# Kernel tuning notes

Hardware: AMD Instinct MI355X
Metric: run time of the kernel (lower is better)

## Reference

```python
import jax, jax.numpy as jnp
import numpy as np

HIDDEN = 2048
N_HEADS = 32
N_KV_HEADS = 8
HEAD_DIM = 64
ROPE_THETA = 500000.0
B, S = 1, 2048


def _rope_tables(seq_len):
    inv_freq = 1.0 / ROPE_THETA ** (jnp.arange(0, HEAD_DIM, 2, dtype=jnp.float32) / HEAD_DIM)
    angles = jnp.arange(seq_len, dtype=jnp.float32)[:, None] * inv_freq[None, :]
    return jnp.cos(angles), jnp.sin(angles)


def _apply_rope(x, cos, sin):
    # x: (B, S, H, D); cos/sin: (S, D//2)
    x1 = x[..., 0::2]
    x2 = x[..., 1::2]
    c = cos[None, :, None, :]
    s = sin[None, :, None, :]
    x1r = x1 * c - x2 * s
    x2r = x1 * s + x2 * c
    return jnp.stack([x1r, x2r], axis=-1).reshape(x.shape)


def setup_inputs() -> dict:
    key = jax.random.key(0)
    ks = jax.random.split(key, 5)
    hidden_states = jax.random.normal(ks[0], (B, S, HIDDEN), dtype=jnp.float32)
    # causal mask, broadcastable over (B, H, S, S)
    attention_mask = jnp.tril(jnp.ones((S, S), dtype=bool))[None, :, :]
    sc = 1.0 / np.sqrt(HIDDEN)
    wq = jax.random.normal(ks[1], (HIDDEN, N_HEADS * HEAD_DIM), dtype=jnp.float32) * sc
    wk = jax.random.normal(ks[2], (HIDDEN, N_KV_HEADS * HEAD_DIM), dtype=jnp.float32) * sc
    wv = jax.random.normal(ks[3], (HIDDEN, N_KV_HEADS * HEAD_DIM), dtype=jnp.float32) * sc
    wo = jax.random.normal(ks[4], (N_HEADS * HEAD_DIM, HIDDEN), dtype=jnp.float32) * sc
    return {"hidden_states": hidden_states, "attention_mask": attention_mask,
            "wq": wq, "wk": wk, "wv": wv, "wo": wo}


def reference(hidden_states, attention_mask, wq, wk, wv, wo):
    b, s, _ = hidden_states.shape
    groups = N_HEADS // N_KV_HEADS
    q = (hidden_states @ wq).reshape(b, s, N_HEADS, HEAD_DIM)
    k = (hidden_states @ wk).reshape(b, s, N_KV_HEADS, HEAD_DIM)
    v = (hidden_states @ wv).reshape(b, s, N_KV_HEADS, HEAD_DIM)
    cos, sin = _rope_tables(s)
    q = _apply_rope(q, cos, sin)
    k = _apply_rope(k, cos, sin)
    k = jnp.repeat(k, groups, axis=2)  # (b, s, H, D)
    v = jnp.repeat(v, groups, axis=2)
    q = q.transpose(0, 2, 1, 3)  # (b, H, s, D)
    k = k.transpose(0, 2, 1, 3)
    v = v.transpose(0, 2, 1, 3)
    scores = jnp.einsum('bhqd,bhkd->bhqk', q, k) / jnp.sqrt(jnp.float32(HEAD_DIM))
    scores = jnp.where(attention_mask[:, None, :, :], scores, -jnp.inf)
    probs = jax.nn.softmax(scores, axis=-1)
    out = jnp.einsum('bhqk,bhkd->bhqd', probs, v)
    out = out.transpose(0, 2, 1, 3).reshape(b, s, N_HEADS * HEAD_DIM)
    return out @ wo
```

## Files before the change

kernel.cpp:

```cpp
#include <hip/hip_runtime.h>

typedef __attribute__((ext_vector_type(8))) short short8;
typedef __attribute__((ext_vector_type(4))) float float4v;

union U4S8 { uint4 u; short8 s; };

__device__ __forceinline__ float bf2f(ushort u) {
    union { uint i; float f; } v; v.i = ((uint)u) << 16; return v.f;
}
__device__ __forceinline__ ushort f2bf(float f) {
    union { uint i; float f; } v; v.f = f;
    return (ushort)((v.i + 0x7FFFu + ((v.i >> 16) & 1u)) >> 16);
}
#if __has_builtin(__builtin_amdgcn_cvt_pk_bf16_f32)
__device__ __forceinline__ uint f2bf_pk(float a, float b) {
    auto r = __builtin_amdgcn_cvt_pk_bf16_f32(a, b);
    return __builtin_bit_cast(uint, r);
}
#else
__device__ __forceinline__ uint f2bf_pk(float a, float b) {
    return (uint)f2bf(a) | ((uint)f2bf(b) << 16);
}
#endif
__device__ __forceinline__ void gld_lds16(const ushort* g, ushort* l) {
    __builtin_amdgcn_global_load_lds((const __attribute__((address_space(1))) unsigned int*)g,
                                     (__attribute__((address_space(3))) unsigned int*)l,
                                     16, 0, 0);
}

__device__ __forceinline__ void tconv_body(const float* in, ushort* out,
                                           int C, int r0, int c0, int tid) {
    __shared__ float t[64][65];
    const int lrow = tid >> 2;
    const int lc   = (tid & 3) * 16;
    const float* ip = in + (size_t)(r0 + lrow) * C + c0 + lc;
#pragma unroll
    for (int i = 0; i < 4; i++) {
        float4 v = *(const float4*)(ip + 4 * i);
        t[lrow][lc + 4 * i + 0] = v.x; t[lrow][lc + 4 * i + 1] = v.y;
        t[lrow][lc + 4 * i + 2] = v.z; t[lrow][lc + 4 * i + 3] = v.w;
    }
    __syncthreads();
    ushort* op = out + (size_t)(c0 + lrow) * 2048 + r0 + lc;
#pragma unroll
    for (int i = 0; i < 8; i++)
        ((uint*)op)[i] = f2bf_pk(t[lc + 2 * i][lrow], t[lc + 2 * i + 1][lrow]);
}

__global__ __launch_bounds__(256) void prep(const float* __restrict__ hidden,
                                            const float* __restrict__ wq,
                                            const float* __restrict__ wk,
                                            const float* __restrict__ wv,
                                            const float* __restrict__ wo,
                                            ushort* __restrict__ hid,
                                            ushort* __restrict__ wT,
                                            ushort* __restrict__ woT) {
    const int bx = blockIdx.x;
    if (bx < 2048) {
        const size_t i = ((size_t)bx * 256 + threadIdx.x) * 8;
        float4 a = *(const float4*)(hidden + i);
        float4 b = *(const float4*)(hidden + i + 4);
        uint4 u;
        u.x = f2bf_pk(a.x, a.y); u.y = f2bf_pk(a.z, a.w);
        u.z = f2bf_pk(b.x, b.y); u.w = f2bf_pk(b.z, b.w);
        *(uint4*)(hid + i) = u;
    } else if (bx < 3584) {
        const int i = bx - 2048;
        const int xx = i % 48, yy = i / 48;
        const float* in; ushort* op; int C, cx;
        if (xx < 32)      { in = wq; op = wT;                        C = 2048; cx = xx; }
        else if (xx < 40) { in = wk; op = wT + (size_t)2048 * 2048;  C = 512;  cx = xx - 32; }
        else              { in = wv; op = wT + (size_t)2560 * 2048;  C = 512;  cx = xx - 40; }
        tconv_body(in, op, C, yy * 64, cx * 64, threadIdx.x);
    } else {
        const int i = bx - 3584;
        tconv_body(wo, woT, 2048, (i >> 5) * 64, (i & 31) * 64, threadIdx.x);
    }
}

template <bool BF16OUT>
__global__ __launch_bounds__(512, 2) void gemm_n128(const ushort* __restrict__ A,
                                                    const ushort* __restrict__ Bt,
                                                    void* __restrict__ Cout,
                                                    int N, int K, int lda, int ropeQKV,
                                                    ushort* __restrict__ VTout) {
    __shared__ ushort As[2][2][128 * 32];
    __shared__ ushort Bs[2][2][128 * 32];

    const int tid = threadIdx.x, w = tid >> 6, lane = tid & 63;
    const int lr = lane & 15, quad = lane >> 4;
    const int m0 = blockIdx.x * 128, n0 = blockIdx.y * 128;
    const int wr = w >> 1, wc = w & 1;

    const int srow = lane >> 2;
    const int skb  = (lane & 3) ^ ((srow >> 1) & 3);

    const ushort* Ap = A  + (size_t)(m0 + 16 * w + srow) * lda + skb * 8;
    const ushort* Bp = Bt + (size_t)(n0 + 16 * w + srow) * K + skb * 8;

    float4v acc[2][4];
#pragma unroll
    for (int a = 0; a < 2; a++)
#pragma unroll
        for (int b = 0; b < 4; b++) { acc[a][b][0] = 0.f; acc[a][b][1] = 0.f; acc[a][b][2] = 0.f; acc[a][b][3] = 0.f; }

    const int fsw = (lr >> 1) & 3;
    const int niter = K >> 6;

    gld_lds16(Ap,      &As[0][0][w * 512]);
    gld_lds16(Ap + 32, &As[0][1][w * 512]);
    gld_lds16(Bp,      &Bs[0][0][w * 512]);
    gld_lds16(Bp + 32, &Bs[0][1][w * 512]);

    for (int it = 0; it < niter; it++) {
        const int b = it & 1;

        asm volatile("s_waitcnt vmcnt(0) lgkmcnt(0)\n\ts_barrier" ::: "memory");

        if (it + 1 < niter) {
            const int k1 = (it + 1) << 6;
            gld_lds16(Ap + k1,      &As[1 - b][0][w * 512]);
            gld_lds16(Ap + k1 + 32, &As[1 - b][1][w * 512]);
            gld_lds16(Bp + k1,      &Bs[1 - b][0][w * 512]);
            gld_lds16(Bp + k1 + 32, &Bs[1 - b][1][w * 512]);
        }

#pragma unroll
        for (int kh = 0; kh < 2; kh++) {
            short8 af[2], bf[4];
#pragma unroll
            for (int mt = 0; mt < 2; mt++)
                af[mt] = *(const short8*)&As[b][kh][(wr * 32 + mt * 16 + lr) * 32 + (quad ^ fsw) * 8];
#pragma unroll
            for (int nt = 0; nt < 4; nt++)
                bf[nt] = *(const short8*)&Bs[b][kh][(wc * 64 + nt * 16 + lr) * 32 + (quad ^ fsw) * 8];
#pragma unroll
            for (int mt = 0; mt < 2; mt++)
#pragma unroll
                for (int nt = 0; nt < 4; nt++)
                    acc[mt][nt] = __builtin_amdgcn_mfma_f32_16x16x32_bf16(af[mt], bf[nt], acc[mt][nt], 0, 0, 0);
        }
    }

    const int rbase = m0 + wr * 32 + quad * 4;
    const int cbase = n0 + wc * 64 + lr;
    if (BF16OUT) {
        ushort* Cb = (ushort*)Cout;
        if (ropeQKV && (int)blockIdx.y >= 20) {
            const int ch = rbase >> 6;
            const int j2 = (wr & 1) * 2;
#pragma unroll
            for (int nt = 0; nt < 4; nt++) {
                const int vd = cbase + nt * 16 - 2560;
                const int vx = vd & 15;
#pragma unroll
                for (int r = 0; r < 4; r++) {
                    const int kl = quad * 4 + r;
                    const uint pk = f2bf_pk(acc[0][nt][r], acc[1][nt][r]);
                    *(uint*)(VTout + (size_t)vd * 2048 + ch * 64
                             + ((kl ^ vx) << 2) + j2) = pk;
                }
            }
        } else if (ropeQKV && (int)blockIdx.y < 20) {
            const float osc = ((int)blockIdx.y < 16) ? 0.18033688f : 1.0f;
            const float sgn = (lr & 1) ? 1.0f : -1.0f;
#pragma unroll
            for (int nt = 0; nt < 4; nt++) {
                const int col = cbase + nt * 16;
                const int j = (col >> 1) & 31;
                const float inv = __expf(-(float)(2 * j) * (1.0f / 64.0f) * 13.122363377404328f);
#pragma unroll
                for (int mt = 0; mt < 2; mt++)
#pragma unroll
                    for (int r = 0; r < 4; r++) {
                        const int row = rbase + mt * 16 + r;
                        float sn, cs;
                        sincosf((float)row * inv, &sn, &cs);
                        const float mine = acc[mt][nt][r];
                        const float partner = __shfl_xor(mine, 1);
                        Cb[(size_t)row * N + col] = f2bf((mine * cs + sgn * partner * sn) * osc);
                    }
            }
        } else {
#pragma unroll
            for (int mt = 0; mt < 2; mt++)
#pragma unroll
                for (int nt = 0; nt < 4; nt++)
#pragma unroll
                    for (int r = 0; r < 4; r++)
                        Cb[(size_t)(rbase + mt * 16 + r) * N + cbase + nt * 16] = f2bf(acc[mt][nt][r]);
        }
    } else {
        float* Cf = (float*)Cout;
#pragma unroll
        for (int mt = 0; mt < 2; mt++)
#pragma unroll
            for (int nt = 0; nt < 4; nt++)
#pragma unroll
                for (int r = 0; r < 4; r++)
                    Cf[(size_t)(rbase + mt * 16 + r) * N + cbase + nt * 16] = acc[mt][nt][r];
    }
}

__global__ __launch_bounds__(256) void attn_mfma(const ushort* __restrict__ Q,
                                                 const ushort* __restrict__ Kc,
                                                 const ushort* __restrict__ VT,
                                                 ushort* __restrict__ O0,
                                                 ushort* __restrict__ O1,
                                                 float* __restrict__ L0,
                                                 float* __restrict__ L1) {
    __shared__ ushort Ks[2][64 * 64];
    __shared__ ushort Vt[2][64 * 64];
    __shared__ ushort Ps[4][16 * 64];

    const int tid = threadIdx.x, w = tid >> 6, lane = tid & 63;
    const int lr = lane & 15, quad = lane >> 4;
    const int h = blockIdx.y, g = h >> 2, z = blockIdx.z;

    const int ksub = lane >> 3, dsub = lane & 7;
    ushort* Pw = Ps[w];
    ushort* Op = z ? O1 : O0;
    float*  Lp = z ? L1 : L0;

    const ushort* Kp0 = Kc + g * 64 + ((dsub ^ ksub) * 8) + (size_t)3072 * ksub;
    const ushort* Vp0 = VT + (size_t)(g * 64 + ksub) * 2048 + dsub * 8;

    short8 onesf;
#pragma unroll
    for (int j = 0; j < 8; j++) onesf[j] = (short)0x3F80;

    for (int ti = 0; ti < 2; ti++) {
        const int bx = ti ? 31 - (int)blockIdx.x : (int)blockIdx.x;
        const int nch = (bx >= z) ? ((bx - z) >> 1) + 1 : 0;

        const ushort* qp = Q + (size_t)(bx * 64 + w * 16 + lr) * 3072 + h * 64 + quad * 8;
        const short8 qf0 = *(const short8*)qp;
        const short8 qf1 = *(const short8*)(qp + 32);

        float4v oacc[4], lacc;
#pragma unroll
        for (int t = 0; t < 4; t++) { oacc[t][0] = 0.f; oacc[t][1] = 0.f; oacc[t][2] = 0.f; oacc[t][3] = 0.f; }
        lacc[0] = 0.f; lacc[1] = 0.f; lacc[2] = 0.f; lacc[3] = 0.f;

        __syncthreads();
        if (nch) {
#pragma unroll
            for (int i = 0; i < 2; i++) {
                const int rt = 2 * w + i;
                gld_lds16(Kp0 + (size_t)(z * 64 + rt * 8) * 3072, &Ks[0][rt * 512]);
                gld_lds16(Vp0 + (size_t)(rt * 8) * 2048 + z * 64, &Vt[0][rt * 512]);
            }
        }

        for (int c = 0; c < nch; c++) {
            const int kb = z + 2 * c;
            const int b = c & 1;
            ushort* bKs = Ks[b];
            ushort* bVt = Vt[b];

            asm volatile("s_waitcnt vmcnt(0) lgkmcnt(0)\n\ts_barrier" ::: "memory");

            if (c + 1 < nch) {
                const int kn = kb + 2;
#pragma unroll
                for (int i = 0; i < 2; i++) {
                    const int rt = 2 * w + i;
                    gld_lds16(Kp0 + (size_t)(kn * 64 + rt * 8) * 3072, &Ks[1 - b][rt * 512]);
                    gld_lds16(Vp0 + (size_t)(rt * 8) * 2048 + kn * 64, &Vt[1 - b][rt * 512]);
                }
            }

            float4v sacc[4];
#pragma unroll
            for (int t = 0; t < 4; t++) { sacc[t][0] = 0.f; sacc[t][1] = 0.f; sacc[t][2] = 0.f; sacc[t][3] = 0.f; }
#pragma unroll
            for (int t = 0; t < 4; t++) {
                const int krow = t * 16 + lr;
                const int sw = lr & 7;
                short8 kf0 = *(const short8*)&bKs[krow * 64 + ((quad)     ^ sw) * 8];
                short8 kf1 = *(const short8*)&bKs[krow * 64 + ((quad + 4) ^ sw) * 8];
                sacc[t] = __builtin_amdgcn_mfma_f32_16x16x32_bf16(qf0, kf0, sacc[t], 0, 0, 0);
                sacc[t] = __builtin_amdgcn_mfma_f32_16x16x32_bf16(qf1, kf1, sacc[t], 0, 0, 0);
            }

            if (kb == bx) {
#pragma unroll
                for (int r = 0; r < 4; r++) {
                    const int qr = w * 16 + quad * 4 + r;
                    float p0 = exp2f(sacc[0][r]), p1 = exp2f(sacc[1][r]);
                    float p2 = exp2f(sacc[2][r]), p3 = exp2f(sacc[3][r]);
                    if (lr > qr)      p0 = 0.f;
                    if (16 + lr > qr) p1 = 0.f;
                    if (32 + lr > qr) p2 = 0.f;
                    if (48 + lr > qr) p3 = 0.f;
                    const int prow = quad * 4 + r;
                    uint2 pk; pk.x = f2bf_pk(p0, p1); pk.y = f2bf_pk(p2, p3);
                    *(uint2*)&Pw[prow * 64 + (lr ^ prow) * 4] = pk;
                }
            } else {
#pragma unroll
                for (int r = 0; r < 4; r++) {
                    const int prow = quad * 4 + r;
                    uint2 pk;
                    pk.x = f2bf_pk(exp2f(sacc[0][r]), exp2f(sacc[1][r]));
                    pk.y = f2bf_pk(exp2f(sacc[2][r]), exp2f(sacc[3][r]));
                    *(uint2*)&Pw[prow * 64 + (lr ^ prow) * 4] = pk;
                }
            }

#pragma unroll
            for (int ks2 = 0; ks2 < 2; ks2++) {
                const int ub = ks2 * 8 + quad * 2;
                U4S8 pu;
                uint2 plo = *(const uint2*)&Pw[lr * 64 + ((ub)     ^ lr) * 4];
                uint2 phi = *(const uint2*)&Pw[lr * 64 + ((ub + 1) ^ lr) * 4];
                pu.u.x = plo.x; pu.u.y = plo.y; pu.u.z = phi.x; pu.u.w = phi.y;
                lacc = __builtin_amdgcn_mfma_f32_16x16x32_bf16(pu.s, onesf, lacc, 0, 0, 0);
#pragma unroll
                for (int t = 0; t < 4; t++) {
                    const int d = t * 16 + lr;
                    U4S8 vu;
                    uint2 vlo = *(const uint2*)&bVt[d * 64 + ((ub)     ^ lr) * 4];
                    uint2 vhi = *(const uint2*)&bVt[d * 64 + ((ub + 1) ^ lr) * 4];
                    vu.u.x = vlo.x; vu.u.y = vlo.y; vu.u.z = vhi.x; vu.u.w = vhi.y;
                    oacc[t] = __builtin_amdgcn_mfma_f32_16x16x32_bf16(pu.s, vu.s, oacc[t], 0, 0, 0);
                }
            }
        }

        ushort* op = Op + (size_t)(bx * 64 + w * 16 + quad * 4) * 2048 + h * 64 + lr;
#pragma unroll
        for (int t = 0; t < 4; t++)
#pragma unroll
            for (int r = 0; r < 4; r++)
                op[(size_t)r * 2048 + t * 16] = f2bf(oacc[t][r]);
        if (lr == 0) {
#pragma unroll
            for (int r = 0; r < 4; r++)
                Lp[h * 2048 + bx * 64 + w * 16 + quad * 4 + r] = lacc[r];
        }
    }
}

__global__ __launch_bounds__(256) void combine(ushort* __restrict__ O0,
                                               const ushort* __restrict__ O1,
                                               const float* __restrict__ L0,
                                               const float* __restrict__ L1) {
    const int idx = blockIdx.x * 256 + threadIdx.x;
    const int r = idx >> 8;
    const int c8 = (idx & 255) * 8;
    const int h = c8 >> 6;
    const float rl = 1.0f / (L0[h * 2048 + r] + L1[h * 2048 + r]);
    uint4 a = *(const uint4*)(O0 + (size_t)r * 2048 + c8);
    uint4 b = *(const uint4*)(O1 + (size_t)r * 2048 + c8);
    uint ua[4] = {a.x, a.y, a.z, a.w}, ub[4] = {b.x, b.y, b.z, b.w};
    uint rr[4];
#pragma unroll
    for (int k = 0; k < 4; k++) {
        float x0 = bf2f((ushort)(ua[k] & 0xFFFFu)) + bf2f((ushort)(ub[k] & 0xFFFFu));
        float x1 = bf2f((ushort)(ua[k] >> 16))     + bf2f((ushort)(ub[k] >> 16));
        rr[k] = f2bf_pk(x0 * rl, x1 * rl);
    }
    uint4 res; res.x = rr[0]; res.y = rr[1]; res.z = rr[2]; res.w = rr[3];
    *(uint4*)(O0 + (size_t)r * 2048 + c8) = res;
}

extern "C" void kernel_launch(void* const* d_in, const int* in_sizes, int n_in,
                              void* d_out, int out_size, void* d_ws, size_t ws_size,
                              hipStream_t stream) {
    const float* hidden = (const float*)d_in[0];
    const float* wq = (const float*)d_in[2];
    const float* wk = (const float*)d_in[3];
    const float* wv = (const float*)d_in[4];
    const float* wo = (const float*)d_in[5];

    ushort* ws = (ushort*)d_ws;
    ushort* hid = ws;
    ushort* wT  = ws + 4194304;
    ushort* woT = ws + 10485760;
    ushort* O1  = wT;
    float*  L0  = (float*)(ws + 8388608);
    float*  L1  = L0 + 65536;
    ushort* QKV = (ushort*)d_out;
    ushort* VT  = QKV + 6291456;

    prep<<<4608, 256, 0, stream>>>(hidden, wq, wk, wv, wo, hid, wT, woT);
    gemm_n128<true><<<dim3(16, 24), 512, 0, stream>>>(hid, wT, QKV, 3072, 2048, 2048, 1, VT);
    attn_mfma<<<dim3(16, 32, 2), 256, 0, stream>>>(QKV, QKV + 2048, VT,
                                                   hid , O1, L0, L1);
    combine<<<2048, 256, 0, stream>>>(hid, O1, L0, L1);
    gemm_n128<false><<<dim3(16, 16), 512, 0, stream>>>(hid, woT, d_out, 2048, 2048, 2048, 0, nullptr);
}
```

Baseline: 233.2 us.

## Fuse split-attention combine into output projection GEMM and use fast exp2

Drops the separate combine kernel. The output-projection GEMM now loads both partial attention outputs and their softmax denominators, merges and normalizes them in registers, and writes the bf16 result into shared memory as the A tile. The B tile is still loaded asynchronously into LDS. This saves one kernel launch and a full read-write round trip of the combined activation, at the cost of reading two A sources per tile in the GEMM with register double-buffering. Separately, exp2f in attention is replaced by the hardware exp2 builtin to avoid extra range handling.

```diff
diff --git a/kernel.cpp b/kernel.cpp
--- a/kernel.cpp
+++ b/kernel.cpp
@@ -21,6 +21,11 @@
 __device__ __forceinline__ uint f2bf_pk(float a, float b) {
     return (uint)f2bf(a) | ((uint)f2bf(b) << 16);
 }
+#endif
+#if __has_builtin(__builtin_amdgcn_exp2f)
+__device__ __forceinline__ float fexp2(float x) { return __builtin_amdgcn_exp2f(x); }
+#else
+__device__ __forceinline__ float fexp2(float x) { return exp2f(x); }
 #endif
 __device__ __forceinline__ void gld_lds16(const ushort* g, ushort* l) {
     __builtin_amdgcn_global_load_lds((const __attribute__((address_space(1))) unsigned int*)g,
@@ -202,6 +207,118 @@
     }
 }
 
+struct ASet { uint4 a0, a1, b0, b1; float l0, l1; };
+
+__device__ __forceinline__ uint4 comb4(uint4 a, uint4 b, float rl) {
+    uint pa[4] = {a.x, a.y, a.z, a.w}, pb[4] = {b.x, b.y, b.z, b.w};
+    uint pr[4];
+#pragma unroll
+    for (int k = 0; k < 4; k++) {
+        float x0 = (bf2f((ushort)(pa[k] & 0xFFFFu)) + bf2f((ushort)(pb[k] & 0xFFFFu))) * rl;
+        float x1 = (bf2f((ushort)(pa[k] >> 16))     + bf2f((ushort)(pb[k] >> 16)))     * rl;
+        pr[k] = f2bf_pk(x0, x1);
+    }
+    uint4 r; r.x = pr[0]; r.y = pr[1]; r.z = pr[2]; r.w = pr[3];
+    return r;
+}
+
+__global__ __launch_bounds__(512, 2) void gemm2_fused(const ushort* __restrict__ O0,
+                                                      const ushort* __restrict__ O1,
+                                                      const float* __restrict__ L0,
+                                                      const float* __restrict__ L1,
+                                                      const ushort* __restrict__ Bt,
+                                                      float* __restrict__ Cout) {
+    __shared__ ushort As[2][2][128 * 32];
+    __shared__ ushort Bs[2][2][128 * 32];
+
+    const int tid = threadIdx.x, w = tid >> 6, lane = tid & 63;
+    const int lr = lane & 15, quad = lane >> 4;
+    const int m0 = blockIdx.x * 128, n0 = blockIdx.y * 128;
+    const int wr = w >> 1, wc = w & 1;
+
+    const int srow = lane >> 2;
+    const int skb  = (lane & 3) ^ ((srow >> 1) & 3);
+    const int arow = m0 + 16 * w + srow;
+
+    const ushort* A0 = O0 + (size_t)arow * 2048 + skb * 8;
+    const ushort* A1 = O1 + (size_t)arow * 2048 + skb * 8;
+    const ushort* Bp = Bt + (size_t)(n0 + 16 * w + srow) * 2048 + skb * 8;
+
+    float4v acc[2][4];
+#pragma unroll
+    for (int a = 0; a < 2; a++)
+#pragma unroll
+        for (int b = 0; b < 4; b++) { acc[a][b][0] = 0.f; acc[a][b][1] = 0.f; acc[a][b][2] = 0.f; acc[a][b][3] = 0.f; }
+
+    const int fsw = (lr >> 1) & 3;
+
+    ASet s0, s1;
+#define LOADSET(S, SLAB)                                                      \
+    if ((SLAB) < 32) {                                                        \
+        const int cb = (SLAB) * 64;                                           \
+        S.a0 = *(const uint4*)(A0 + cb);      S.a1 = *(const uint4*)(A0 + cb + 32); \
+        S.b0 = *(const uint4*)(A1 + cb);      S.b1 = *(const uint4*)(A1 + cb + 32); \
+        S.l0 = L0[(SLAB) * 2048 + arow];      S.l1 = L1[(SLAB) * 2048 + arow];      \
+    }
+#define WRITESET(S, BUF)                                                      \
+    {                                                                         \
+        const float rl = 1.0f / (S.l0 + S.l1);                                \
+        *(uint4*)&As[BUF][0][w * 512 + lane * 8] = comb4(S.a0, S.b0, rl);     \
+        *(uint4*)&As[BUF][1][w * 512 + lane * 8] = comb4(S.a1, S.b1, rl);     \
+    }
+#define GSTEP2(IT, B, SW, SL)                                                 \
+    {                                                                         \
+        asm volatile("s_waitcnt vmcnt(0) lgkmcnt(0)\n\ts_barrier" ::: "memory"); \
+        if ((IT) + 1 < 32) {                                                  \
+            WRITESET(SW, 1 - (B));                                            \
+            const int k1 = ((IT) + 1) << 6;                                   \
+            gld_lds16(Bp + k1,      &Bs[1 - (B)][0][w * 512]);                \
+            gld_lds16(Bp + k1 + 32, &Bs[1 - (B)][1][w * 512]);                \
+        }                                                                     \
+        LOADSET(SL, (IT) + 2);                                                \
+        _Pragma("unroll")                                                     \
+        for (int kh = 0; kh < 2; kh++) {                                      \
+            short8 af[2], bf[4];                                              \
+            _Pragma("unroll")                                                 \
+            for (int mt = 0; mt < 2; mt++)                                    \
+                af[mt] = *(const short8*)&As[B][kh][(wr * 32 + mt * 16 + lr) * 32 + (quad ^ fsw) * 8]; \
+            _Pragma("unroll")                                                 \
+            for (int nt = 0; nt < 4; nt++)                                    \
+                bf[nt] = *(const short8*)&Bs[B][kh][(wc * 64 + nt * 16 + lr) * 32 + (quad ^ fsw) * 8]; \
+            _Pragma("unroll")                                                 \
+            for (int mt = 0; mt < 2; mt++)                                    \
+                _Pragma("unroll")                                             \
+                for (int nt = 0; nt < 4; nt++)                                \
+                    acc[mt][nt] = __builtin_amdgcn_mfma_f32_16x16x32_bf16(af[mt], bf[nt], acc[mt][nt], 0, 0, 0); \
+        }                                                                     \
+    }
+
+    LOADSET(s0, 0)
+    LOADSET(s1, 1)
+    gld_lds16(Bp,      &Bs[0][0][w * 512]);
+    gld_lds16(Bp + 32, &Bs[0][1][w * 512]);
+    asm volatile("s_waitcnt vmcnt(0)" ::: "memory");
+    WRITESET(s0, 0)
+
+    for (int i2 = 0; i2 < 16; i2++) {
+        GSTEP2(2 * i2,     0, s1, s0)
+        GSTEP2(2 * i2 + 1, 1, s0, s1)
+    }
+#undef GSTEP2
+#undef WRITESET
+#undef LOADSET
+
+    const int rbase = m0 + wr * 32 + quad * 4;
+    const int cbase = n0 + wc * 64 + lr;
+#pragma unroll
+    for (int mt = 0; mt < 2; mt++)
+#pragma unroll
+        for (int nt = 0; nt < 4; nt++)
+#pragma unroll
+            for (int r = 0; r < 4; r++)
+                Cout[(size_t)(rbase + mt * 16 + r) * 2048 + cbase + nt * 16] = acc[mt][nt][r];
+}
+
 __global__ __launch_bounds__(256) void attn_mfma(const ushort* __restrict__ Q,
                                                  const ushort* __restrict__ Kc,
                                                  const ushort* __restrict__ VT,
@@ -287,8 +404,8 @@
 #pragma unroll
                 for (int r = 0; r < 4; r++) {
                     const int qr = w * 16 + quad * 4 + r;
-                    float p0 = exp2f(sacc[0][r]), p1 = exp2f(sacc[1][r]);
-                    float p2 = exp2f(sacc[2][r]), p3 = exp2f(sacc[3][r]);
+                    float p0 = fexp2(sacc[0][r]), p1 = fexp2(sacc[1][r]);
+                    float p2 = fexp2(sacc[2][r]), p3 = fexp2(sacc[3][r]);
                     if (lr > qr)      p0 = 0.f;
                     if (16 + lr > qr) p1 = 0.f;
                     if (32 + lr > qr) p2 = 0.f;
@@ -302,8 +419,8 @@
                 for (int r = 0; r < 4; r++) {
                     const int prow = quad * 4 + r;
                     uint2 pk;
-                    pk.x = f2bf_pk(exp2f(sacc[0][r]), exp2f(sacc[1][r]));
-                    pk.y = f2bf_pk(exp2f(sacc[2][r]), exp2f(sacc[3][r]));
+                    pk.x = f2bf_pk(fexp2(sacc[0][r]), fexp2(sacc[1][r]));
+                    pk.y = f2bf_pk(fexp2(sacc[2][r]), fexp2(sacc[3][r]));
                     *(uint2*)&Pw[prow * 64 + (lr ^ prow) * 4] = pk;
                 }
             }
@@ -340,29 +457,6 @@
                 Lp[h * 2048 + bx * 64 + w * 16 + quad * 4 + r] = lacc[r];
         }
     }
-}
-
-__global__ __launch_bounds__(256) void combine(ushort* __restrict__ O0,
-                                               const ushort* __restrict__ O1,
-                                               const float* __restrict__ L0,
-                                               const float* __restrict__ L1) {
-    const int idx = blockIdx.x * 256 + threadIdx.x;
-    const int r = idx >> 8;
-    const int c8 = (idx & 255) * 8;
-    const int h = c8 >> 6;
-    const float rl = 1.0f / (L0[h * 2048 + r] + L1[h * 2048 + r]);
-    uint4 a = *(const uint4*)(O0 + (size_t)r * 2048 + c8);
-    uint4 b = *(const uint4*)(O1 + (size_t)r * 2048 + c8);
-    uint ua[4] = {a.x, a.y, a.z, a.w}, ub[4] = {b.x, b.y, b.z, b.w};
-    uint rr[4];
-#pragma unroll
-    for (int k = 0; k < 4; k++) {
-        float x0 = bf2f((ushort)(ua[k] & 0xFFFFu)) + bf2f((ushort)(ub[k] & 0xFFFFu));
-        float x1 = bf2f((ushort)(ua[k] >> 16))     + bf2f((ushort)(ub[k] >> 16));
-        rr[k] = f2bf_pk(x0 * rl, x1 * rl);
-    }
-    uint4 res; res.x = rr[0]; res.y = rr[1]; res.z = rr[2]; res.w = rr[3];
-    *(uint4*)(O0 + (size_t)r * 2048 + c8) = res;
 }
 
 extern "C" void kernel_launch(void* const* d_in, const int* in_sizes, int n_in,
@@ -388,6 +482,5 @@
     gemm_n128<true><<<dim3(16, 24), 512, 0, stream>>>(hid, wT, QKV, 3072, 2048, 2048, 1, VT);
     attn_mfma<<<dim3(16, 32, 2), 256, 0, stream>>>(QKV, QKV + 2048, VT,
                                                    hid , O1, L0, L1);
-    combine<<<2048, 256, 0, stream>>>(hid, O1, L0, L1);
-    gemm_n128<false><<<dim3(16, 16), 512, 0, stream>>>(hid, woT, d_out, 2048, 2048, 2048, 0, nullptr);
-}
+    gemm2_fused<<<dim3(16, 16), 512, 0, stream>>>(hid, O1, L0, L1, woT, (float*)d_out);
+}
```

Measured after the change: 236.3 us. No clear change (+1.3%).
